# Kernel tuning notes

Hardware: AMD Instinct MI355X
Metric: run time of the kernel (lower is better)

Reference implementation:

```python
import jax, jax.numpy as jnp
import numpy as np

B, IN_DIM, HID = 8192, 1024, 1024

def setup_inputs() -> dict:
    key = jax.random.key(0)
    ks = jax.random.split(key, 11)
    s_in = 1.0 / np.sqrt(IN_DIM + HID)  # torch Linear default init scale
    inp = {
        "Z": jax.random.normal(ks[0], (B, IN_DIM), dtype=jnp.float32),
        "h_prev": jax.random.normal(ks[1], (B, HID), dtype=jnp.float32),
        "c_prev": jax.random.normal(ks[2], (B, HID), dtype=jnp.float32),
        "W_i": jax.random.uniform(ks[3], (IN_DIM + HID, HID), jnp.float32, -s_in, s_in),
        "b_i": jax.random.uniform(ks[4], (HID,), jnp.float32, -s_in, s_in),
        "W_f": jax.random.uniform(ks[5], (IN_DIM + HID, HID), jnp.float32, -s_in, s_in),
        "b_f": jax.random.uniform(ks[6], (HID,), jnp.float32, -s_in, s_in),
        "W_o": jax.random.uniform(ks[7], (IN_DIM + HID, HID), jnp.float32, -s_in, s_in),
        "b_o": jax.random.uniform(ks[8], (HID,), jnp.float32, -s_in, s_in),
        "W_g": jax.random.uniform(ks[9], (IN_DIM + HID, HID), jnp.float32, -s_in, s_in),
        "b_g": jax.random.uniform(ks[10], (HID,), jnp.float32, -s_in, s_in),
    }
    return inp

def reference(Z, h_prev, c_prev, W_i, b_i, W_f, b_f, W_o, b_o, W_g, b_g):
    combined = jnp.concatenate([Z, h_prev], axis=1)  # [B, IN+HID]
    i = jax.nn.sigmoid(combined @ W_i + b_i)
    f = jax.nn.sigmoid(combined @ W_f + b_f)
    o = jax.nn.sigmoid(combined @ W_o + b_o)
    g = jnp.tanh(combined @ W_g + b_g)
    c = f * c_prev + i * g
    h = o * jnp.tanh(c)
    return (h, c)
```

## Files before the change

kernel.cpp:

```cpp
#include <hip/hip_runtime.h>


#define BDIM 8192
#define KDIM 2048
#define NDIM 1024
#define NCAT 4096

typedef __bf16 bf16x8 __attribute__((ext_vector_type(8)));
typedef __bf16 bf16x4 __attribute__((ext_vector_type(4)));
typedef float  f32x4  __attribute__((ext_vector_type(4)));

__device__ __forceinline__ void async_cp16(const void* g, void* l) {
    __builtin_amdgcn_global_load_lds((__attribute__((address_space(1))) void*)g,
                                     (__attribute__((address_space(3))) void*)l,
                                     16, 0, 0);
}

__device__ __forceinline__ float sigm(float x) { return 1.f / (1.f + __expf(-x)); }
__device__ __forceinline__ float tanh_fast(float x) { return 1.f - 2.f / (1.f + __expf(2.f * x)); }

__global__ void prep_kernel(const float* __restrict__ Z, const float* __restrict__ H,
                            const float* __restrict__ Wi, const float* __restrict__ Wf,
                            const float* __restrict__ Wo, const float* __restrict__ Wg,
                            __bf16* __restrict__ A, __bf16* __restrict__ Wt) {
    __shared__ float t[32][33];
    int bid = blockIdx.x;
    if (bid < 16384) {
        int idx = bid * 256 + threadIdx.x;
        int row = idx >> 9;
        int q   = idx & 511;
        float4 v;
        if (q < 256) v = ((const float4*)Z)[row * 256 + q];
        else         v = ((const float4*)H)[row * 256 + (q - 256)];
        bf16x4 o = { (__bf16)v.x, (__bf16)v.y, (__bf16)v.z, (__bf16)v.w };
        ((bf16x4*)A)[idx] = o;
    } else {
        int id  = bid - 16384;
        int g   = id >> 11;
        int rem = id & 2047;
        int k0  = (rem & 63) * 32;
        int n0  = (rem >> 6) * 32;
        const float* W = (g == 0) ? Wi : (g == 1) ? Wf : (g == 2) ? Wo : Wg;
        int c = threadIdx.x & 31, r8 = threadIdx.x >> 5;
        #pragma unroll
        for (int j = 0; j < 4; ++j) {
            int r = r8 + j * 8;
            t[r][c] = W[(size_t)(k0 + r) * NDIM + (n0 + c)];
        }
        __syncthreads();
        size_t outRow = (size_t)((n0 >> 5) * 128 + g * 32);
        #pragma unroll
        for (int j = 0; j < 4; ++j) {
            int r = r8 + j * 8;
            Wt[(outRow + r) * KDIM + (k0 + c)] = (__bf16)t[c][r];
        }
    }
}

__global__ __launch_bounds__(256, 3)
void lstm_gemm_kernel(const __bf16* __restrict__ A, const __bf16* __restrict__ Wt,
                      const float* __restrict__ b_i, const float* __restrict__ b_f,
                      const float* __restrict__ b_o, const float* __restrict__ b_g,
                      const float* __restrict__ c_prev, float* __restrict__ out) {
    __shared__ char smem[33792];
    __bf16* As = (__bf16*)smem;
    __bf16* Bs = (__bf16*)(smem + 8192);
    float*  Ep = (float*)smem;

    const int tid  = threadIdx.x;
    const int wave = tid >> 6;
    const int lane = tid & 63;
    const int wr = wave >> 1, wc = wave & 1;
    const int bx = blockIdx.x;
    const int m0 = blockIdx.y * 128;
    const int ncat0 = bx * 128;

    const int srow   = lane >> 2;
    const int schunk = (lane & 3) ^ ((lane >> 3) & 3);
    const __bf16* Ag[2]; __bf16* Al[2];
    const __bf16* Bg[2]; __bf16* Bl[2];
    #pragma unroll
    for (int i = 0; i < 2; ++i) {
        int grp = wave * 2 + i;
        Ag[i] = A  + (size_t)(m0    + grp * 16 + srow) * KDIM + schunk * 8;
        Bg[i] = Wt + (size_t)(ncat0 + grp * 16 + srow) * KDIM + schunk * 8;
        Al[i] = As + grp * 512;
        Bl[i] = Bs + grp * 512;
    }

    const int l15  = lane & 15;
    const int quad = lane >> 4;
    const int ksw  = (quad ^ ((l15 >> 1) & 3)) * 8;
    int aoff[4], boff[4];
    #pragma unroll
    for (int t = 0; t < 4; ++t) {
        aoff[t] = (wr * 64 + t * 16 + l15) * 32 + ksw;
        boff[t] = (wc * 64 + t * 16 + l15) * 32 + ksw;
    }

    f32x4 acc[4][4];
    #pragma unroll
    for (int i = 0; i < 4; ++i)
        #pragma unroll
        for (int j = 0; j < 4; ++j) acc[i][j] = (f32x4){0.f, 0.f, 0.f, 0.f};

    for (int k0 = 0; k0 < KDIM; k0 += 32) {
        async_cp16(Ag[0] + k0, Al[0]);
        async_cp16(Ag[1] + k0, Al[1]);
        async_cp16(Bg[0] + k0, Bl[0]);
        async_cp16(Bg[1] + k0, Bl[1]);
        __syncthreads();

        bf16x8 af[4], bfr[4];
        #pragma unroll
        for (int t = 0; t < 4; ++t) af[t]  = *(const bf16x8*)(As + aoff[t]);
        #pragma unroll
        for (int t = 0; t < 4; ++t) bfr[t] = *(const bf16x8*)(Bs + boff[t]);

        #pragma unroll
        for (int mt = 0; mt < 4; ++mt)
            #pragma unroll
            for (int nt = 0; nt < 4; ++nt)
                acc[mt][nt] = __builtin_amdgcn_mfma_f32_16x16x32_bf16(af[mt], bfr[nt], acc[mt][nt], 0, 0, 0);
        __syncthreads();
    }

    const float* bias_lo = (wc == 0) ? b_i : b_o;
    const float* bias_hi = (wc == 0) ? b_f : b_g;
    float bv[4];
    bv[0] = bias_lo[bx * 32 + l15];
    bv[1] = bias_lo[bx * 32 + 16 + l15];
    bv[2] = bias_hi[bx * 32 + l15];
    bv[3] = bias_hi[bx * 32 + 16 + l15];

    #pragma unroll
    for (int c = 0; c < 2; ++c) {
        __syncthreads();
        if (wr == c) {
            #pragma unroll
            for (int mt = 0; mt < 4; ++mt)
                #pragma unroll
                for (int nt = 0; nt < 4; ++nt)
                    #pragma unroll
                    for (int r = 0; r < 4; ++r)
                        Ep[(mt * 16 + quad * 4 + r) * 132 + wc * 64 + nt * 16 + l15] =
                            acc[mt][nt][r] + bv[nt];
        }
        __syncthreads();

        #pragma unroll
        for (int e = 0; e < 8; ++e) {
            int idx = tid + e * 256;
            int row = idx >> 5, n = idx & 31;
            float gi = sigm(Ep[row * 132 + n]);
            float gf = sigm(Ep[row * 132 + 32 + n]);
            float go = sigm(Ep[row * 132 + 64 + n]);
            float gg = tanh_fast(Ep[row * 132 + 96 + n]);
            size_t pos = (size_t)(m0 + c * 64 + row) * NDIM + bx * 32 + n;
            float cp = c_prev[pos];
            float cv = gf * cp + gi * gg;
            out[pos] = go * tanh_fast(cv);
            out[(size_t)BDIM * NDIM + pos] = cv;
        }
    }
}

extern "C" void kernel_launch(void* const* d_in, const int* in_sizes, int n_in,
                              void* d_out, int out_size, void* d_ws, size_t ws_size,
                              hipStream_t stream) {
    const float* Z  = (const float*)d_in[0];
    const float* H  = (const float*)d_in[1];
    const float* Cp = (const float*)d_in[2];
    const float* Wi = (const float*)d_in[3];
    const float* bi = (const float*)d_in[4];
    const float* Wf = (const float*)d_in[5];
    const float* bf = (const float*)d_in[6];
    const float* Wo = (const float*)d_in[7];
    const float* bo = (const float*)d_in[8];
    const float* Wg = (const float*)d_in[9];
    const float* bg = (const float*)d_in[10];

    __bf16* Acomb = (__bf16*)d_ws;
    __bf16* Wt    = (__bf16*)((char*)d_ws + (size_t)33554432);

    prep_kernel<<<16384 + 8192, 256, 0, stream>>>(Z, H, Wi, Wf, Wo, Wg, Acomb, Wt);
    lstm_gemm_kernel<<<dim3(NCAT / 128, BDIM / 128), 256, 0, stream>>>(
        Acomb, Wt, bi, bf, bo, bg, Cp, (float*)d_out);
}
```

Before: 341.9 us.

## Double K-step per barrier, swizzle block order, shrink epilogue staging for occupancy

The GEMM main loop now loads two 32-wide K slices per iteration, which halves the number of barrier pairs per K, and shared memory for the A/B tiles is doubled to 16KB each. Block IDs are remapped onto a 1D grid so that groups of blocks sharing the same A rows run together, which is meant to improve L2 reuse. The epilogue is split into four 32-row passes so its staging buffer fits in 32KB, and launch bounds are raised to 4 blocks per CU. The cost is more epilogue barriers and possible register pressure under the higher occupancy target.

```diff
diff --git a/kernel.cpp b/kernel.cpp
--- a/kernel.cpp
+++ b/kernel.cpp
@@ -57,22 +57,25 @@
     }
 }
 
-__global__ __launch_bounds__(256, 3)
+__global__ __launch_bounds__(256, 4)
 void lstm_gemm_kernel(const __bf16* __restrict__ A, const __bf16* __restrict__ Wt,
                       const float* __restrict__ b_i, const float* __restrict__ b_f,
                       const float* __restrict__ b_o, const float* __restrict__ b_g,
                       const float* __restrict__ c_prev, float* __restrict__ out) {
-    __shared__ char smem[33792];
+    __shared__ char smem[32768];
     __bf16* As = (__bf16*)smem;
-    __bf16* Bs = (__bf16*)(smem + 8192);
+    __bf16* Bs = (__bf16*)(smem + 16384);
     float*  Ep = (float*)smem;
 
     const int tid  = threadIdx.x;
     const int wave = tid >> 6;
     const int lane = tid & 63;
     const int wr = wave >> 1, wc = wave & 1;
-    const int bx = blockIdx.x;
-    const int m0 = blockIdx.y * 128;
+
+    const int bid = blockIdx.x;
+    const int bx = (bid & 7) * 4 + ((bid >> 3) & 3);
+    const int by = bid >> 5;
+    const int m0 = by * 128;
     const int ncat0 = bx * 128;
 
     const int srow   = lane >> 2;
@@ -104,24 +107,29 @@
         #pragma unroll
         for (int j = 0; j < 4; ++j) acc[i][j] = (f32x4){0.f, 0.f, 0.f, 0.f};
 
-    for (int k0 = 0; k0 < KDIM; k0 += 32) {
-        async_cp16(Ag[0] + k0, Al[0]);
-        async_cp16(Ag[1] + k0, Al[1]);
-        async_cp16(Bg[0] + k0, Bl[0]);
-        async_cp16(Bg[1] + k0, Bl[1]);
+    for (int k0 = 0; k0 < KDIM; k0 += 64) {
+        #pragma unroll
+        for (int h = 0; h < 2; ++h)
+            #pragma unroll
+            for (int i = 0; i < 2; ++i) {
+                async_cp16(Ag[i] + k0 + h * 32, Al[i] + h * 4096);
+                async_cp16(Bg[i] + k0 + h * 32, Bl[i] + h * 4096);
+            }
         __syncthreads();
 
-        bf16x8 af[4], bfr[4];
         #pragma unroll
-        for (int t = 0; t < 4; ++t) af[t]  = *(const bf16x8*)(As + aoff[t]);
-        #pragma unroll
-        for (int t = 0; t < 4; ++t) bfr[t] = *(const bf16x8*)(Bs + boff[t]);
-
-        #pragma unroll
-        for (int mt = 0; mt < 4; ++mt)
+        for (int h = 0; h < 2; ++h) {
+            bf16x8 af[4], bfr[4];
             #pragma unroll
-            for (int nt = 0; nt < 4; ++nt)
-                acc[mt][nt] = __builtin_amdgcn_mfma_f32_16x16x32_bf16(af[mt], bfr[nt], acc[mt][nt], 0, 0, 0);
+            for (int t = 0; t < 4; ++t) af[t]  = *(const bf16x8*)(As + h * 4096 + aoff[t]);
+            #pragma unroll
+            for (int t = 0; t < 4; ++t) bfr[t] = *(const bf16x8*)(Bs + h * 4096 + boff[t]);
+            #pragma unroll
+            for (int mt = 0; mt < 4; ++mt)
+                #pragma unroll
+                for (int nt = 0; nt < 4; ++nt)
+                    acc[mt][nt] = __builtin_amdgcn_mfma_f32_16x16x32_bf16(af[mt], bfr[nt], acc[mt][nt], 0, 0, 0);
+        }
         __syncthreads();
     }
 
@@ -134,29 +142,31 @@
     bv[3] = bias_hi[bx * 32 + 16 + l15];
 
     #pragma unroll
-    for (int c = 0; c < 2; ++c) {
+    for (int c = 0; c < 4; ++c) {
         __syncthreads();
-        if (wr == c) {
+        if (wr == (c >> 1)) {
             #pragma unroll
-            for (int mt = 0; mt < 4; ++mt)
+            for (int mi = 0; mi < 2; ++mi) {
+                int mt = (c & 1) * 2 + mi;
                 #pragma unroll
                 for (int nt = 0; nt < 4; ++nt)
                     #pragma unroll
                     for (int r = 0; r < 4; ++r)
-                        Ep[(mt * 16 + quad * 4 + r) * 132 + wc * 64 + nt * 16 + l15] =
+                        Ep[(mi * 16 + quad * 4 + r) * 132 + wc * 64 + nt * 16 + l15] =
                             acc[mt][nt][r] + bv[nt];
+            }
         }
         __syncthreads();
 
         #pragma unroll
-        for (int e = 0; e < 8; ++e) {
+        for (int e = 0; e < 4; ++e) {
             int idx = tid + e * 256;
             int row = idx >> 5, n = idx & 31;
             float gi = sigm(Ep[row * 132 + n]);
             float gf = sigm(Ep[row * 132 + 32 + n]);
             float go = sigm(Ep[row * 132 + 64 + n]);
             float gg = tanh_fast(Ep[row * 132 + 96 + n]);
-            size_t pos = (size_t)(m0 + c * 64 + row) * NDIM + bx * 32 + n;
+            size_t pos = (size_t)(m0 + c * 32 + row) * NDIM + bx * 32 + n;
             float cp = c_prev[pos];
             float cv = gf * cp + gi * gg;
             out[pos] = go * tanh_fast(cv);
@@ -184,6 +194,6 @@
     __bf16* Wt    = (__bf16*)((char*)d_ws + (size_t)33554432);
 
     prep_kernel<<<16384 + 8192, 256, 0, stream>>>(Z, H, Wi, Wf, Wo, Wg, Acomb, Wt);
-    lstm_gemm_kernel<<<dim3(NCAT / 128, BDIM / 128), 256, 0, stream>>>(
+    lstm_gemm_kernel<<<dim3(NCAT / 128 * BDIM / 128), 256, 0, stream>>>(
         Acomb, Wt, bi, bf, bo, bg, Cp, (float*)d_out);
 }
```

Result: faster. 331.8 us (-3.0%).
